# Optimization experiments

Measured on AMD Instinct MI355X. Metric: run time of the kernel, lower is better.

## Reference

```python
import jax, jax.numpy as jnp
import numpy as np

N = 8192
N_DIM = 7
N_WIDTH = 64


def setup_inputs() -> dict:
    key = jax.random.key(0)
    ks = jax.random.split(key, 12)
    scale = 0.05
    u = lambda k, shape: scale * (2.0 * jax.random.uniform(k, shape) - 1.0)
    # Linear params stored as (in, out) so forward uses x @ W + b (same math as torch Linear).
    lin = lambda k, fan_in, fan_out: (
        jax.random.uniform(jax.random.fold_in(k, 0), (fan_in, fan_out),
                           minval=-1.0, maxval=1.0) / np.sqrt(fan_in),
        jax.random.uniform(jax.random.fold_in(k, 1), (fan_out,),
                           minval=-1.0, maxval=1.0) / np.sqrt(fan_in),
    )
    W1, b1 = lin(ks[1], N_DIM, N_WIDTH)
    W2, b2 = lin(ks[2], N_WIDTH, N_WIDTH)
    Wl, bl = lin(ks[3], N_WIDTH, 1)
    return {
        "x": jax.random.normal(ks[0], (N, N_DIM), dtype=jnp.float32),
        "alpha": jax.random.uniform(ks[4], (1,)),          # Edges.alpha = 1 * rand(1)
        "W1": W1, "b1": b1, "wt1": u(ks[5], (N_WIDTH, N_WIDTH)), "bs1": u(ks[6], (1,)),
        "W2": W2, "b2": b2, "wt2": u(ks[7], (N_WIDTH, N_WIDTH)), "bs2": u(ks[8], (1,)),
        "Wl": Wl, "bl": bl,
    }


def _edges(x, alpha):
    eta, phi = x[:, 1], x[:, 2]
    deta = eta[:, None] - eta[None, :]                      # (n, n)
    dphi = jnp.abs(phi[:, None] - phi[None, :])
    dphi = jnp.where(dphi > jnp.pi, 2.0 * jnp.pi - dphi, dphi)
    dRdR = deta * deta + dphi * dphi
    A = jnp.exp(-alpha[0] * dRdR)
    return jax.nn.softmax(A, axis=1) + jnp.eye(x.shape[0], dtype=x.dtype)


def _gcn_layer(X, A, W, b, wt, bs):
    X = jax.nn.relu(X @ W + b)                              # embed + relu
    X = (A @ X) @ wt + bs[0]                                # aggregate + mix + scalar bias
    return jax.nn.relu(X)


def reference(x, alpha, W1, b1, wt1, bs1, W2, b2, wt2, bs2, Wl, bl):
    A = _edges(x, alpha)
    V = jax.nn.relu(_gcn_layer(x, A, W1, b1, wt1, bs1))
    V = jax.nn.relu(_gcn_layer(V, A, W2, b2, wt2, bs2))
    s = V.sum(axis=0)                                       # (n_width,)
    return jax.nn.sigmoid(s @ Wl + bl)                      # (1,)
```

## Files before the change

### kernel.cpp

```cpp
#include <hip/hip_runtime.h>
#include <math.h>

#define NN 8192
#define L2E 1.44269504088896340736f
#define TWO_PI 6.28318530717958647693f

typedef _Float16 h8 __attribute__((ext_vector_type(8)));
typedef _Float16 h4 __attribute__((ext_vector_type(4)));
typedef float f32x4 __attribute__((ext_vector_type(4)));
typedef float f32x2 __attribute__((ext_vector_type(2)));
typedef unsigned int u32x4 __attribute__((ext_vector_type(4)));
#define MFMA16(A, B, C) __builtin_amdgcn_mfma_f32_16x16x32_f16(A, B, C, 0, 0, 0)

#define GLD_LDS16(gsrc, ldst)                                          \
  __builtin_amdgcn_global_load_lds(                                    \
      (const __attribute__((address_space(1))) unsigned int*)(gsrc),   \
      (__attribute__((address_space(3))) unsigned int*)(ldst), 16, 0, 0)

union V8 { float4 v[2]; float f[8]; };

__global__ __launch_bounds__(256) void prep_kernel(
    const float* __restrict__ x, const float* __restrict__ alpha,
    const float* __restrict__ W1, const float* __restrict__ b1,
    float* __restrict__ eta_s, float* __restrict__ phi_s,
    float* __restrict__ H1, _Float16* __restrict__ HT1,
    float* __restrict__ svec)
{
  __shared__ float sW[448];
  __shared__ float sb[64];
  __shared__ float T[32][68];
  const int t = threadIdx.x;
  if (blockIdx.x == 0 && t < 64) svec[t] = 0.f;
  for (int k = t; k < 448; k += 256) sW[k] = W1[k];
  if (t < 64) sb[t] = b1[t];
  const float s = sqrtf(alpha[0] * L2E);
  const int i0 = blockIdx.x * 32;
  const int r = t >> 3, q = t & 7;
  const int i = i0 + r;
  float xv[7];
#pragma unroll
  for (int k = 0; k < 7; k++) xv[k] = x[i * 7 + k];
  if (q == 0) { eta_s[i] = xv[1] * s; phi_s[i] = xv[2] * s; }
  __syncthreads();
#pragma unroll
  for (int c = 0; c < 8; c++) {
    const int n = q * 8 + c;
    float hv = sb[n];
#pragma unroll
    for (int k = 0; k < 7; k++) hv = fmaf(xv[k], sW[k * 64 + n], hv);
    T[r][n] = fmaxf(hv, 0.f);
  }
  __syncthreads();
  for (int e = t; e < 512; e += 256)
    *(f32x4*)(H1 + (size_t)i0 * 64 + (e << 2)) =
        *(const f32x4*)&T[e >> 4][(e << 2) & 63];
  const int n = t >> 2, sg = (t & 3) * 8;
  h8 v;
#pragma unroll
  for (int ss = 0; ss < 8; ss++) v[ss] = (_Float16)T[sg + ss][n];
  *(h8*)(HT1 + (size_t)n * NN + i0 + sg) = v;
}

template <bool PASS1>
__global__ __launch_bounds__(256, 4) void attn_pass(
    const float* __restrict__ eta_s, const float* __restrict__ phi_s,
    const _Float16* __restrict__ HT, const float* __restrict__ alpha,
    unsigned char* __restrict__ Pm8,
    float* __restrict__ Ypart, float* __restrict__ lpart)
{
  __shared__ __align__(16) char smem[32768];
  _Float16* stage = (_Float16*)smem;
  const int tid = threadIdx.x;
  const int w = tid >> 6, lane = tid & 63, m = lane & 15, g = lane >> 4;
  const int tile = blockIdx.x >> 2, part = blockIdx.x & 3;
  const int i0 = tile << 5;
  const int jbase = part << 11;
  const int jcol0 = jbase + (w << 5) + (g << 3);

  const int r0 = tid >> 4, gq = tid & 15;
  const _Float16* sbase = HT + (size_t)r0 * NN + ((gq ^ r0) << 3) + jbase;

  f32x4 a00 = {0,0,0,0}, a01 = {0,0,0,0}, a02 = {0,0,0,0}, a03 = {0,0,0,0};
  f32x4 a10 = {0,0,0,0}, a11 = {0,0,0,0}, a12 = {0,0,0,0}, a13 = {0,0,0,0};
  f32x4 l0a = {0,0,0,0}, l1a = {0,0,0,0};
  const h8 onesv = {(_Float16)1.f, (_Float16)1.f, (_Float16)1.f, (_Float16)1.f,
                    (_Float16)1.f, (_Float16)1.f, (_Float16)1.f, (_Float16)1.f};

  unsigned char* const pfb8 =
      Pm8 + ((size_t)blockIdx.x * 16) * 4096 + (w << 10) + (lane << 4);

  float Cs = 0.f, et0 = 0.f, ph0 = 0.f, et1 = 0.f, ph1 = 0.f;
  const float* ep = nullptr;
  const float* pp = nullptr;
  V8 E0, P0, E1, P1;
  u32x4 pe8, po8;
  if constexpr (PASS1) {
    Cs = TWO_PI * sqrtf(alpha[0] * L2E);
    et0 = eta_s[i0 + m];      ph0 = phi_s[i0 + m];
    et1 = eta_s[i0 + 16 + m]; ph1 = phi_s[i0 + 16 + m];
    ep = eta_s + jcol0;
    pp = phi_s + jcol0;
    E0.v[0] = *(const float4*)ep;  E0.v[1] = *(const float4*)(ep + 4);
    P0.v[0] = *(const float4*)pp;  P0.v[1] = *(const float4*)(pp + 4);
  } else {
    pe8 = *(const u32x4*)(pfb8);
    po8 = *(const u32x4*)(pfb8 + 4096);
  }

#pragma unroll
  for (int k = 0; k < 4; ++k)
    GLD_LDS16(sbase + (size_t)k * 16 * NN, stage + ((k * 256 + tid) << 3));
  __syncthreads();

  const int fs = ((m << 4) + (((w << 2) | g) ^ m)) << 3;

  union AF { h8 v; decltype(__builtin_amdgcn_cvt_pkrtz(0.f, 0.f)) p[4]; };

  auto stage_compute = [&](const V8& Ec, const V8& Pc, const _Float16* cur,
                           int sIdx) {
    const h8 b0 = *(const h8*)(cur + fs);
    const h8 b1 = *(const h8*)(cur + 2048 + fs);
    const h8 b2 = *(const h8*)(cur + 4096 + fs);
    const h8 b3 = *(const h8*)(cur + 6144 + fs);
    AF af0, af1;
    float pva[8], pvb[8];
#pragma unroll
    for (int tt = 0; tt < 8; tt += 2) {
      const f32x2 pj = {Pc.f[tt], Pc.f[tt + 1]};
      const f32x2 ej = {Ec.f[tt], Ec.f[tt + 1]};
      const f32x2 dp0 = ph0 - pj, dp1 = ph1 - pj;
      const f32x2 ad0 = {fabsf(dp0.x), fabsf(dp0.y)};
      const f32x2 ad1 = {fabsf(dp1.x), fabsf(dp1.y)};
      const f32x2 cm0 = Cs - ad0, cm1 = Cs - ad1;
      const f32x2 wr0 = {fminf(ad0.x, cm0.x), fminf(ad0.y, cm0.y)};
      const f32x2 wr1 = {fminf(ad1.x, cm1.x), fminf(ad1.y, cm1.y)};
      const f32x2 de0 = et0 - ej, de1 = et1 - ej;
      const f32x2 r20 = de0 * de0 + wr0 * wr0;
      const f32x2 r21 = de1 * de1 + wr1 * wr1;
      const f32x2 ax0 = {__builtin_amdgcn_exp2f(-r20.x),
                         __builtin_amdgcn_exp2f(-r20.y)};
      const f32x2 ax1 = {__builtin_amdgcn_exp2f(-r21.x),
                         __builtin_amdgcn_exp2f(-r21.y)};
      const f32x2 ga0 = ax0 * L2E - L2E;
      const f32x2 ga1 = ax1 * L2E - L2E;
      const float va0 = __builtin_amdgcn_exp2f(ga0.x);
      const float va1 = __builtin_amdgcn_exp2f(ga0.y);
      const float vb0 = __builtin_amdgcn_exp2f(ga1.x);
      const float vb1 = __builtin_amdgcn_exp2f(ga1.y);
      pva[tt] = va0; pva[tt + 1] = va1;
      pvb[tt] = vb0; pvb[tt + 1] = vb1;
      af0.p[tt >> 1] = __builtin_amdgcn_cvt_pkrtz(va0, va1);
      af1.p[tt >> 1] = __builtin_amdgcn_cvt_pkrtz(vb0, vb1);
    }
    unsigned int ra0 = __builtin_amdgcn_cvt_pk_fp8_f32(pva[0], pva[1], 0, false);
    ra0 = __builtin_amdgcn_cvt_pk_fp8_f32(pva[2], pva[3], ra0, true);
    unsigned int ra1 = __builtin_amdgcn_cvt_pk_fp8_f32(pva[4], pva[5], 0, false);
    ra1 = __builtin_amdgcn_cvt_pk_fp8_f32(pva[6], pva[7], ra1, true);
    unsigned int rb0 = __builtin_amdgcn_cvt_pk_fp8_f32(pvb[0], pvb[1], 0, false);
    rb0 = __builtin_amdgcn_cvt_pk_fp8_f32(pvb[2], pvb[3], rb0, true);
    unsigned int rb1 = __builtin_amdgcn_cvt_pk_fp8_f32(pvb[4], pvb[5], 0, false);
    rb1 = __builtin_amdgcn_cvt_pk_fp8_f32(pvb[6], pvb[7], rb1, true);
    const u32x4 r8 = {ra0, ra1, rb0, rb1};
    *(u32x4*)(pfb8 + sIdx * 4096) = r8;
    __builtin_amdgcn_s_setprio(1);
    a00 = MFMA16(af0.v, b0, a00); a01 = MFMA16(af0.v, b1, a01);
    a02 = MFMA16(af0.v, b2, a02); a03 = MFMA16(af0.v, b3, a03);
    a10 = MFMA16(af1.v, b0, a10); a11 = MFMA16(af1.v, b1, a11);
    a12 = MFMA16(af1.v, b2, a12); a13 = MFMA16(af1.v, b3, a13);
    l0a = MFMA16(af0.v, onesv, l0a);
    l1a = MFMA16(af1.v, onesv, l1a);
    __builtin_amdgcn_s_setprio(0);
  };

  auto stage_gemm = [&](u32x4 r8, const _Float16* cur) {
    const h8 b0 = *(const h8*)(cur + fs);
    const h8 b1 = *(const h8*)(cur + 2048 + fs);
    const h8 b2 = *(const h8*)(cur + 4096 + fs);
    const h8 b3 = *(const h8*)(cur + 6144 + fs);
    AF af0, af1;
    {
      const f32x2 c01 = __builtin_amdgcn_cvt_pk_f32_fp8(r8.x, false);
      const f32x2 c23 = __builtin_amdgcn_cvt_pk_f32_fp8(r8.x, true);
      const f32x2 c45 = __builtin_amdgcn_cvt_pk_f32_fp8(r8.y, false);
      const f32x2 c67 = __builtin_amdgcn_cvt_pk_f32_fp8(r8.y, true);
      af0.p[0] = __builtin_amdgcn_cvt_pkrtz(c01.x, c01.y);
      af0.p[1] = __builtin_amdgcn_cvt_pkrtz(c23.x, c23.y);
      af0.p[2] = __builtin_amdgcn_cvt_pkrtz(c45.x, c45.y);
      af0.p[3] = __builtin_amdgcn_cvt_pkrtz(c67.x, c67.y);
    }
    {
      const f32x2 c01 = __builtin_amdgcn_cvt_pk_f32_fp8(r8.z, false);
      const f32x2 c23 = __builtin_amdgcn_cvt_pk_f32_fp8(r8.z, true);
      const f32x2 c45 = __builtin_amdgcn_cvt_pk_f32_fp8(r8.w, false);
      const f32x2 c67 = __builtin_amdgcn_cvt_pk_f32_fp8(r8.w, true);
      af1.p[0] = __builtin_amdgcn_cvt_pkrtz(c01.x, c01.y);
      af1.p[1] = __builtin_amdgcn_cvt_pkrtz(c23.x, c23.y);
      af1.p[2] = __builtin_amdgcn_cvt_pkrtz(c45.x, c45.y);
      af1.p[3] = __builtin_amdgcn_cvt_pkrtz(c67.x, c67.y);
    }
    __builtin_amdgcn_s_setprio(1);
    a00 = MFMA16(af0.v, b0, a00); a01 = MFMA16(af0.v, b1, a01);
    a02 = MFMA16(af0.v, b2, a02); a03 = MFMA16(af0.v, b3, a03);
    a10 = MFMA16(af1.v, b0, a10); a11 = MFMA16(af1.v, b1, a11);
    a12 = MFMA16(af1.v, b2, a12); a13 = MFMA16(af1.v, b3, a13);
    __builtin_amdgcn_s_setprio(0);
  };

#pragma unroll
  for (int s2 = 0; s2 < 8; ++s2) {
    {
      const _Float16* src = sbase + (2 * s2 + 1) * 128;
#pragma unroll
      for (int k = 0; k < 4; ++k)
        GLD_LDS16(src + (size_t)k * 16 * NN,
                  stage + 8192 + ((k * 256 + tid) << 3));
      if constexpr (PASS1) {
        E1.v[0] = *(const float4*)(ep + s2 * 256 + 128);
        E1.v[1] = *(const float4*)(ep + s2 * 256 + 132);
        P1.v[0] = *(const float4*)(pp + s2 * 256 + 128);
        P1.v[1] = *(const float4*)(pp + s2 * 256 + 132);
        stage_compute(E0, P0, stage, 2 * s2);
      } else {
        const u32x4 c = pe8;
        if (s2 < 7) {
          pe8 = *(const u32x4*)(pfb8 + (2 * s2 + 2) * 4096);
        }
        stage_gemm(c, stage);
      }
      __syncthreads();
    }
    {
      if (s2 < 7) {
        const _Float16* src = sbase + (2 * s2 + 2) * 128;
#pragma unroll
        for (int k = 0; k < 4; ++k)
          GLD_LDS16(src + (size_t)k * 16 * NN,
                    stage + ((k * 256 + tid) << 3));
        if constexpr (PASS1) {
          E0.v[0] = *(const float4*)(ep + s2 * 256 + 256);
          E0.v[1] = *(const float4*)(ep + s2 * 256 + 260);
          P0.v[0] = *(const float4*)(pp + s2 * 256 + 256);
          P0.v[1] = *(const float4*)(pp + s2 * 256 + 260);
        }
      }
      if constexpr (PASS1) {
        stage_compute(E1, P1, stage + 8192, 2 * s2 + 1);
      } else {
        const u32x4 c = po8;
        if (s2 < 7) {
          po8 = *(const u32x4*)(pfb8 + (2 * s2 + 3) * 4096);
        }
        stage_gemm(c, stage + 8192);
      }
      __syncthreads();
    }
  }

  typedef float Red2[32][66];
  Red2* red = (Red2*)smem;
  const int h = w >> 1;
  if ((w & 1) == 0) {
#pragma unroll
    for (int r = 0; r < 4; ++r) {
      red[h][g * 4 + r][m]      = a00[r]; red[h][g * 4 + r][16 + m] = a01[r];
      red[h][g * 4 + r][32 + m] = a02[r]; red[h][g * 4 + r][48 + m] = a03[r];
      red[h][16 + g * 4 + r][m]      = a10[r]; red[h][16 + g * 4 + r][16 + m] = a11[r];
      red[h][16 + g * 4 + r][32 + m] = a12[r]; red[h][16 + g * 4 + r][48 + m] = a13[r];
    }
    if constexpr (PASS1) {
      if (m == 0) {
#pragma unroll
        for (int r = 0; r < 4; ++r) {
          red[h][g * 4 + r][64]      = l0a[r];
          red[h][16 + g * 4 + r][64] = l1a[r];
        }
      }
    }
  }
  __syncthreads();
  if (w & 1) {
#pragma unroll
    for (int r = 0; r < 4; ++r) {
      red[h][g * 4 + r][m]      += a00[r]; red[h][g * 4 + r][16 + m] += a01[r];
      red[h][g * 4 + r][32 + m] += a02[r]; red[h][g * 4 + r][48 + m] += a03[r];
      red[h][16 + g * 4 + r][m]      += a10[r]; red[h][16 + g * 4 + r][16 + m] += a11[r];
      red[h][16 + g * 4 + r][32 + m] += a12[r]; red[h][16 + g * 4 + r][48 + m] += a13[r];
    }
    if constexpr (PASS1) {
      if (m == 0) {
#pragma unroll
        for (int r = 0; r < 4; ++r) {
          red[h][g * 4 + r][64]      += l0a[r];
          red[h][16 + g * 4 + r][64] += l1a[r];
        }
      }
    }
  }
  __syncthreads();
#pragma unroll
  for (int k = 0; k < 8; ++k) {
    const int e = tid + k * 256;
    Ypart[((size_t)part * NN + i0 + (e >> 6)) * 64 + (e & 63)] =
        red[0][e >> 6][e & 63] + red[1][e >> 6][e & 63];
  }
  if constexpr (PASS1) {
    if (tid < 32)
      lpart[(size_t)part * NN + i0 + tid] = red[0][tid][64] + red[1][tid][64];
  }
}

__global__ __launch_bounds__(256) void mid_kernel(
    const float* __restrict__ Yp, const float* __restrict__ lp,
    const float* __restrict__ H1, const float* __restrict__ wt1,
    const float* __restrict__ bs1, const float* __restrict__ W2,
    const float* __restrict__ b2, float* __restrict__ H2,
    _Float16* __restrict__ HT2)
{
  __shared__ float sA[64][68];
  __shared__ float sB[64][68];
  __shared__ float U[16][68];
  __shared__ float sb2v[64];
  const int t = threadIdx.x;
  for (int e = t; e < 1024; e += 256) {
    const int rr = e >> 4, cc = (e << 2) & 63;
    *(f32x4*)&sA[rr][cc] = *(const f32x4*)(wt1 + (e << 2));
    *(f32x4*)&sB[rr][cc] = *(const f32x4*)(W2 + (e << 2));
  }
  if (t < 64) sb2v[t] = b2[t];
  const float bsv = bs1[0];
  const int i0 = blockIdx.x * 16;
  const int r = t >> 4, q = t & 15;
  const int i = i0 + r;
  float l = 0.f;
#pragma unroll
  for (int p = 0; p < 4; ++p) l += lp[(size_t)p * NN + i];
  const float rl = 1.0f / l;
  f32x4 ya = {0, 0, 0, 0};
#pragma unroll
  for (int p = 0; p < 4; ++p)
    ya += *(const f32x4*)(Yp + ((size_t)p * NN + i) * 64 + q * 4);
  const f32x4 h1 = *(const f32x4*)(H1 + (size_t)i * 64 + q * 4);
#pragma unroll
  for (int c = 0; c < 4; ++c) U[r][q * 4 + c] = fmaf(ya[c], rl, h1[c]);
  __syncthreads();
  float z[4];
#pragma unroll
  for (int c = 0; c < 4; ++c) z[c] = bsv;
#pragma unroll
  for (int k4 = 0; k4 < 64; k4 += 4) {
    const f32x4 u4 = *(const f32x4*)&U[r][k4];
#pragma unroll
    for (int kk = 0; kk < 4; ++kk) {
      const f32x4 sa = *(const f32x4*)&sA[k4 + kk][q * 4];
#pragma unroll
      for (int c = 0; c < 4; ++c) z[c] = fmaf(u4[kk], sa[c], z[c]);
    }
  }
  __syncthreads();
#pragma unroll
  for (int c = 0; c < 4; ++c) U[r][q * 4 + c] = fmaxf(z[c], 0.f);
  __syncthreads();
  float hv[4];
#pragma unroll
  for (int c = 0; c < 4; ++c) hv[c] = sb2v[q * 4 + c];
#pragma unroll
  for (int k4 = 0; k4 < 64; k4 += 4) {
    const f32x4 u4 = *(const f32x4*)&U[r][k4];
#pragma unroll
    for (int kk = 0; kk < 4; ++kk) {
      const f32x4 sb4 = *(const f32x4*)&sB[k4 + kk][q * 4];
#pragma unroll
      for (int c = 0; c < 4; ++c) hv[c] = fmaf(u4[kk], sb4[c], hv[c]);
    }
  }
  __syncthreads();
#pragma unroll
  for (int c = 0; c < 4; ++c) U[r][q * 4 + c] = fmaxf(hv[c], 0.f);
  __syncthreads();
  *(f32x4*)(H2 + (size_t)i0 * 64 + (t << 2)) =
      *(const f32x4*)&U[t >> 4][(t << 2) & 63];
  const int n = t >> 2, sg = (t & 3) * 4;
  h4 v;
#pragma unroll
  for (int ss = 0; ss < 4; ss++) v[ss] = (_Float16)U[sg + ss][n];
  *(h4*)(HT2 + (size_t)n * NN + i0 + sg) = v;
}

__global__ __launch_bounds__(256) void final_kernel(
    const float* __restrict__ Yp, const float* __restrict__ lp,
    const float* __restrict__ H2, const float* __restrict__ wt2,
    const float* __restrict__ bs2, float* __restrict__ svec)
{
  __shared__ float sA[64][68];
  __shared__ float U[16][68];
  __shared__ float cred[4][64];
  const int t = threadIdx.x;
  for (int e = t; e < 1024; e += 256) {
    const int rr = e >> 4, cc = (e << 2) & 63;
    *(f32x4*)&sA[rr][cc] = *(const f32x4*)(wt2 + (e << 2));
  }
  const float bsv = bs2[0];
  const int i0 = blockIdx.x * 16;
  const int r = t >> 4, q = t & 15;
  const int i = i0 + r;
  float l = 0.f;
#pragma unroll
  for (int p = 0; p < 4; ++p) l += lp[(size_t)p * NN + i];
  const float rl = 1.0f / l;
  f32x4 ya = {0, 0, 0, 0};
#pragma unroll
  for (int p = 0; p < 4; ++p)
    ya += *(const f32x4*)(Yp + ((size_t)p * NN + i) * 64 + q * 4);
  const f32x4 h2 = *(const f32x4*)(H2 + (size_t)i * 64 + q * 4);
#pragma unroll
  for (int c = 0; c < 4; ++c) U[r][q * 4 + c] = fmaf(ya[c], rl, h2[c]);
  __syncthreads();
  float z[4];
#pragma unroll
  for (int c = 0; c < 4; ++c) z[c] = bsv;
#pragma unroll
  for (int k4 = 0; k4 < 64; k4 += 4) {
    const f32x4 u4 = *(const f32x4*)&U[r][k4];
#pragma unroll
    for (int kk = 0; kk < 4; ++kk) {
      const f32x4 sa = *(const f32x4*)&sA[k4 + kk][q * 4];
#pragma unroll
      for (int c = 0; c < 4; ++c) z[c] = fmaf(u4[kk], sa[c], z[c]);
    }
  }
  __syncthreads();
#pragma unroll
  for (int c = 0; c < 4; ++c) U[r][q * 4 + c] = fmaxf(z[c], 0.f);
  __syncthreads();
  const int col = t & 63, rg = t >> 6;
  float ps = 0.f;
#pragma unroll
  for (int rr = 0; rr < 4; rr++) ps += U[rg * 4 + rr][col];
  cred[rg][col] = ps;
  __syncthreads();
  if (t < 64)
    atomicAdd(svec + t, cred[0][t] + cred[1][t] + cred[2][t] + cred[3][t]);
}

__global__ void out_kernel(const float* __restrict__ svec,
                           const float* __restrict__ Wl,
                           const float* __restrict__ bl,
                           float* __restrict__ out)
{
  const int t = threadIdx.x;
  float v = svec[t] * Wl[t];
#pragma unroll
  for (int off = 32; off > 0; off >>= 1) v += __shfl_down(v, off);
  if (t == 0) {
    const float logit = v + bl[0];
    out[0] = 1.0f / (1.0f + __builtin_amdgcn_exp2f(-logit * L2E));
  }
}

extern "C" void kernel_launch(void* const* d_in, const int* in_sizes, int n_in,
                              void* d_out, int out_size, void* d_ws,
                              size_t ws_size, hipStream_t stream)
{
  const float* x     = (const float*)d_in[0];
  const float* alpha = (const float*)d_in[1];
  const float* W1    = (const float*)d_in[2];
  const float* b1    = (const float*)d_in[3];
  const float* wt1   = (const float*)d_in[4];
  const float* bs1   = (const float*)d_in[5];
  const float* W2    = (const float*)d_in[6];
  const float* b2    = (const float*)d_in[7];
  const float* wt2   = (const float*)d_in[8];
  const float* bs2   = (const float*)d_in[9];
  const float* Wl    = (const float*)d_in[10];
  const float* bl    = (const float*)d_in[11];
  float* out = (float*)d_out;

  char* ws = (char*)d_ws;
  size_t off = 0;
  auto alloc = [&](size_t bytes) {
    void* p = ws + off;
    off = (off + bytes + 255) & ~(size_t)255;
    return p;
  };
  float* eta_s = (float*)alloc(NN * 4 + 256);
  float* phi_s = (float*)alloc(NN * 4 + 256);
  float* H1    = (float*)alloc((size_t)NN * 64 * 4);
  float* H2    = (float*)alloc((size_t)NN * 64 * 4);
  float* Ypart = (float*)alloc((size_t)4 * NN * 64 * 4);
  float* lpart = (float*)alloc((size_t)4 * NN * 4);
  _Float16* HT = (_Float16*)alloc((size_t)NN * 64 * 2 + 512);
  float* svec  = (float*)alloc(64 * 4);
  unsigned char* Pm8 = (unsigned char*)alloc((size_t)NN * NN);

  prep_kernel<<<256, 256, 0, stream>>>(x, alpha, W1, b1, eta_s, phi_s, H1, HT, svec);
  attn_pass<true><<<1024, 256, 0, stream>>>(eta_s, phi_s, HT, alpha, Pm8, Ypart, lpart);
  mid_kernel<<<512, 256, 0, stream>>>(Ypart, lpart, H1, wt1, bs1, W2, b2, H2, HT);
  attn_pass<false><<<1024, 256, 0, stream>>>(eta_s, phi_s, HT, alpha, Pm8, Ypart, nullptr);
  final_kernel<<<512, 256, 0, stream>>>(Ypart, lpart, H2, wt2, bs2, svec);
  out_kernel<<<1, 64, 0, stream>>>(svec, Wl, bl, out);
}
```

Measured before the change: 157.9 us.

## Deepen LDS staging to four buffers and process two stages per barrier

Grows the attention kernel's LDS staging area from two to four 16KB buffers. Each loop iteration now prefetches the next two K-slabs while computing the current two, which halves the number of __syncthreads barriers and doubles how far ahead loads are issued. In exchange it doubles shared memory per block and lowers the launch-bounds occupancy hint from 4 to 2 blocks per CU, so fewer waves are available to hide latency. It also keeps more prefetched eta/phi or fp8 values live in registers.

```diff
diff --git a/kernel.cpp b/kernel.cpp
--- a/kernel.cpp
+++ b/kernel.cpp
@@ -62,14 +62,14 @@
 }
 
 template <bool PASS1>
-__global__ __launch_bounds__(256, 4) void attn_pass(
+__global__ __launch_bounds__(256, 2) void attn_pass(
     const float* __restrict__ eta_s, const float* __restrict__ phi_s,
     const _Float16* __restrict__ HT, const float* __restrict__ alpha,
     unsigned char* __restrict__ Pm8,
     float* __restrict__ Ypart, float* __restrict__ lpart)
 {
-  __shared__ __align__(16) char smem[32768];
-  _Float16* stage = (_Float16*)smem;
+  __shared__ __align__(16) char smem[65536];
+  _Float16* const stage = (_Float16*)smem;
   const int tid = threadIdx.x;
   const int w = tid >> 6, lane = tid & 63, m = lane & 15, g = lane >> 4;
   const int tile = blockIdx.x >> 2, part = blockIdx.x & 3;
@@ -89,27 +89,34 @@
   unsigned char* const pfb8 =
       Pm8 + ((size_t)blockIdx.x * 16) * 4096 + (w << 10) + (lane << 4);
 
+  auto soff = [](int t) { return (((t >> 1) & 1) << 14) | ((t & 1) << 13); };
+
   float Cs = 0.f, et0 = 0.f, ph0 = 0.f, et1 = 0.f, ph1 = 0.f;
   const float* ep = nullptr;
   const float* pp = nullptr;
-  V8 E0, P0, E1, P1;
-  u32x4 pe8, po8;
+  V8 Ec0, Pc0, Ec1, Pc1, En0, Pn0, En1, Pn1;
+  u32x4 c80, c81, n80, n81;
   if constexpr (PASS1) {
     Cs = TWO_PI * sqrtf(alpha[0] * L2E);
     et0 = eta_s[i0 + m];      ph0 = phi_s[i0 + m];
     et1 = eta_s[i0 + 16 + m]; ph1 = phi_s[i0 + 16 + m];
     ep = eta_s + jcol0;
     pp = phi_s + jcol0;
-    E0.v[0] = *(const float4*)ep;  E0.v[1] = *(const float4*)(ep + 4);
-    P0.v[0] = *(const float4*)pp;  P0.v[1] = *(const float4*)(pp + 4);
+    Ec0.v[0] = *(const float4*)ep;          Ec0.v[1] = *(const float4*)(ep + 4);
+    Pc0.v[0] = *(const float4*)pp;          Pc0.v[1] = *(const float4*)(pp + 4);
+    Ec1.v[0] = *(const float4*)(ep + 128);  Ec1.v[1] = *(const float4*)(ep + 132);
+    Pc1.v[0] = *(const float4*)(pp + 128);  Pc1.v[1] = *(const float4*)(pp + 132);
   } else {
-    pe8 = *(const u32x4*)(pfb8);
-    po8 = *(const u32x4*)(pfb8 + 4096);
-  }
-
-#pragma unroll
-  for (int k = 0; k < 4; ++k)
-    GLD_LDS16(sbase + (size_t)k * 16 * NN, stage + ((k * 256 + tid) << 3));
+    c80 = *(const u32x4*)(pfb8);
+    c81 = *(const u32x4*)(pfb8 + 4096);
+  }
+
+#pragma unroll
+  for (int t = 0; t < 2; ++t)
+#pragma unroll
+    for (int k = 0; k < 4; ++k)
+      GLD_LDS16(sbase + t * 128 + (size_t)k * 16 * NN,
+                stage + soff(t) + ((k * 256 + tid) << 3));
   __syncthreads();
 
   const int fs = ((m << 4) + (((w << 2) | g) ^ m)) << 3;
@@ -207,53 +214,42 @@
   };
 
 #pragma unroll
-  for (int s2 = 0; s2 < 8; ++s2) {
-    {
-      const _Float16* src = sbase + (2 * s2 + 1) * 128;
-#pragma unroll
-      for (int k = 0; k < 4; ++k)
-        GLD_LDS16(src + (size_t)k * 16 * NN,
-                  stage + 8192 + ((k * 256 + tid) << 3));
-      if constexpr (PASS1) {
-        E1.v[0] = *(const float4*)(ep + s2 * 256 + 128);
-        E1.v[1] = *(const float4*)(ep + s2 * 256 + 132);
-        P1.v[0] = *(const float4*)(pp + s2 * 256 + 128);
-        P1.v[1] = *(const float4*)(pp + s2 * 256 + 132);
-        stage_compute(E0, P0, stage, 2 * s2);
-      } else {
-        const u32x4 c = pe8;
-        if (s2 < 7) {
-          pe8 = *(const u32x4*)(pfb8 + (2 * s2 + 2) * 4096);
-        }
-        stage_gemm(c, stage);
-      }
-      __syncthreads();
-    }
-    {
-      if (s2 < 7) {
-        const _Float16* src = sbase + (2 * s2 + 2) * 128;
+  for (int sb = 0; sb < 8; ++sb) {
+    const int s0 = 2 * sb, s1 = 2 * sb + 1;
+    if (sb < 7) {
+#pragma unroll
+      for (int t = 0; t < 2; ++t) {
+        const int ts = s0 + 2 + t;
+        const _Float16* src = sbase + ts * 128;
 #pragma unroll
         for (int k = 0; k < 4; ++k)
           GLD_LDS16(src + (size_t)k * 16 * NN,
-                    stage + ((k * 256 + tid) << 3));
-        if constexpr (PASS1) {
-          E0.v[0] = *(const float4*)(ep + s2 * 256 + 256);
-          E0.v[1] = *(const float4*)(ep + s2 * 256 + 260);
-          P0.v[0] = *(const float4*)(pp + s2 * 256 + 256);
-          P0.v[1] = *(const float4*)(pp + s2 * 256 + 260);
-        }
+                    stage + soff(ts) + ((k * 256 + tid) << 3));
       }
       if constexpr (PASS1) {
-        stage_compute(E1, P1, stage + 8192, 2 * s2 + 1);
+        En0.v[0] = *(const float4*)(ep + (s0 + 2) * 128);
+        En0.v[1] = *(const float4*)(ep + (s0 + 2) * 128 + 4);
+        Pn0.v[0] = *(const float4*)(pp + (s0 + 2) * 128);
+        Pn0.v[1] = *(const float4*)(pp + (s0 + 2) * 128 + 4);
+        En1.v[0] = *(const float4*)(ep + (s1 + 2) * 128);
+        En1.v[1] = *(const float4*)(ep + (s1 + 2) * 128 + 4);
+        Pn1.v[0] = *(const float4*)(pp + (s1 + 2) * 128);
+        Pn1.v[1] = *(const float4*)(pp + (s1 + 2) * 128 + 4);
       } else {
-        const u32x4 c = po8;
-        if (s2 < 7) {
-          po8 = *(const u32x4*)(pfb8 + (2 * s2 + 3) * 4096);
-        }
-        stage_gemm(c, stage + 8192);
+        n80 = *(const u32x4*)(pfb8 + (s0 + 2) * 4096);
+        n81 = *(const u32x4*)(pfb8 + (s1 + 2) * 4096);
       }
-      __syncthreads();
-    }
+    }
+    if constexpr (PASS1) {
+      stage_compute(Ec0, Pc0, stage + soff(s0), s0);
+      stage_compute(Ec1, Pc1, stage + soff(s1), s1);
+      Ec0 = En0; Pc0 = Pn0; Ec1 = En1; Pc1 = Pn1;
+    } else {
+      stage_gemm(c80, stage + soff(s0));
+      stage_gemm(c81, stage + soff(s1));
+      c80 = n80; c81 = n81;
+    }
+    __syncthreads();
   }
 
   typedef float Red2[32][66];
```

Measured after the change: 163.2 us. 3.4% more time.
